# Optimization experiments

Measured on AMD Instinct MI355X. Metric: run time of the kernel, lower is better.

Reference implementation:

```python
import jax, jax.numpy as jnp
import numpy as np

D_MODEL = 1024
N_HEADS = 16
HEAD_DIM = D_MODEL // N_HEADS
FF_DIM = 4096
EPS = 1e-5


def _layer_norm(v, g, b):
    mu = jnp.mean(v, axis=-1, keepdims=True)
    var = jnp.mean(jnp.square(v - mu), axis=-1, keepdims=True)
    return (v - mu) * jax.lax.rsqrt(var + EPS) * g + b


def setup_inputs() -> dict:
    key = jax.random.key(0)
    ks = jax.random.split(key, 16)
    s = 0.02
    x = jax.random.normal(ks[0], (2, 2048, D_MODEL), dtype=jnp.float32)
    Wq = jax.random.normal(ks[1], (D_MODEL, D_MODEL), dtype=jnp.float32) * s
    Wk = jax.random.normal(ks[2], (D_MODEL, D_MODEL), dtype=jnp.float32) * s
    Wv = jax.random.normal(ks[3], (D_MODEL, D_MODEL), dtype=jnp.float32) * s
    Wo = jax.random.normal(ks[4], (D_MODEL, D_MODEL), dtype=jnp.float32) * s
    bq = jnp.zeros((D_MODEL,), jnp.float32)
    bk = jnp.zeros((D_MODEL,), jnp.float32)
    bv = jnp.zeros((D_MODEL,), jnp.float32)
    bo = jnp.zeros((D_MODEL,), jnp.float32)
    # per-head Conv1d(kernel=1) == per-head linear; weights [H, out, in]
    W1 = jax.random.normal(ks[5], (N_HEADS, FF_DIM, HEAD_DIM), dtype=jnp.float32) * s
    b1 = jnp.zeros((N_HEADS, FF_DIM), jnp.float32)
    W2 = jax.random.normal(ks[6], (N_HEADS, HEAD_DIM, FF_DIM), dtype=jnp.float32) * s
    b2 = jnp.zeros((N_HEADS, HEAD_DIM), jnp.float32)
    g1 = jnp.ones((D_MODEL,), jnp.float32)
    be1 = jnp.zeros((D_MODEL,), jnp.float32)
    g2 = jnp.ones((D_MODEL,), jnp.float32)
    be2 = jnp.zeros((D_MODEL,), jnp.float32)
    return {"x": x, "Wq": Wq, "bq": bq, "Wk": Wk, "bk": bk, "Wv": Wv, "bv": bv,
            "Wo": Wo, "bo": bo, "W1": W1, "b1": b1, "W2": W2, "b2": b2,
            "g1": g1, "be1": be1, "g2": g2, "be2": be2}


def reference(x, Wq, bq, Wk, bk, Wv, bv, Wo, bo, W1, b1, W2, b2, g1, be1, g2, be2):
    B, S, D = x.shape
    H, hd = N_HEADS, HEAD_DIM
    # --- multi-head self-attention (standard scaled dot-product) ---
    q = (x @ Wq + bq).reshape(B, S, H, hd)
    k = (x @ Wk + bk).reshape(B, S, H, hd)
    v = (x @ Wv + bv).reshape(B, S, H, hd)
    scores = jnp.einsum('bqhd,bkhd->bhqk', q, k) / jnp.sqrt(jnp.float32(hd))
    attn = jax.nn.softmax(scores, axis=-1)          # [B,H,S,S]
    ctx = jnp.einsum('bhqk,bkhd->bqhd', attn, v).reshape(B, S, D)
    residual = ctx @ Wo + bo
    # dropout is identity in eval mode
    x1 = _layer_norm(x + residual, g1, be1)
    # --- per-head feed-forward (Conv1d kernel=1 per head, batched over heads) ---
    xh = x1.reshape(B, S, H, hd)
    h = jax.nn.relu(jnp.einsum('bshd,hfd->bshf', xh, W1) + b1)   # [B,S,H,FF]
    ff = jnp.einsum('bshf,hdf->bshd', h, W2) + b2                 # [B,S,H,hd]
    y = _layer_norm(x1 + ff.reshape(B, S, D), g2, be2)
    return (y, attn)
```

## Files before the change

kernel.cpp:

```cpp
#include <hip/hip_runtime.h>
#include <cstddef>

#define D_M 1024
#define NH 16
#define HD 64
#define FFD 4096
#define SQ 2048
#define BB 2
#define TOK (BB*SQ)
#define EPS 1e-5f

typedef __attribute__((ext_vector_type(8))) short bf16x8;
typedef __attribute__((ext_vector_type(4))) float f32x4;

__device__ inline unsigned short f32_bf16_rne(float f) {
  unsigned int u = __float_as_uint(f);
  unsigned int r = (u + 0x7fffu + ((u >> 16) & 1u)) >> 16;
  return (unsigned short)r;
}

__device__ inline float wave_sum(float v) {
  #pragma unroll
  for (int m = 32; m >= 1; m >>= 1) v += __shfl_xor(v, m);
  return v;
}

__global__ __launch_bounds__(256)
void convert_bf16_k(const float* __restrict__ src, unsigned short* __restrict__ dst, int n4) {
  int i = blockIdx.x * 256 + threadIdx.x;
  if (i >= n4) return;
  float4 v = ((const float4*)src)[i];
  ushort4 h;
  h.x = f32_bf16_rne(v.x); h.y = f32_bf16_rne(v.y);
  h.z = f32_bf16_rne(v.z); h.w = f32_bf16_rne(v.w);
  ((ushort4*)dst)[i] = h;
}

__global__ __launch_bounds__(256)
void transp4_k(const float* __restrict__ W0, const float* __restrict__ W1_,
               const float* __restrict__ W2_, const float* __restrict__ W3,
               unsigned short* __restrict__ h0, unsigned short* __restrict__ h1,
               unsigned short* __restrict__ h2, unsigned short* __restrict__ h3) {
  const float* W; unsigned short* hT;
  switch (blockIdx.z) {
    case 0: W = W0; hT = h0; break;
    case 1: W = W1_; hT = h1; break;
    case 2: W = W2_; hT = h2; break;
    default: W = W3; hT = h3; break;
  }
  __shared__ float tile[64][65];
  const int bn = blockIdx.x * 64;
  const int bk = blockIdx.y * 64;
  const int t = threadIdx.x;
  #pragma unroll
  for (int i = 0; i < 4; ++i) {
    int r = (t >> 4) + i * 16, c = (t & 15) * 4;
    float4 v = *(const float4*)&W[(size_t)(bk + r) * D_M + bn + c];
    tile[r][c] = v.x; tile[r][c + 1] = v.y; tile[r][c + 2] = v.z; tile[r][c + 3] = v.w;
  }
  __syncthreads();
  #pragma unroll
  for (int i = 0; i < 4; ++i) {
    int n = (t >> 4) + i * 16, k = (t & 15) * 4;
    ushort4 h;
    h.x = f32_bf16_rne(tile[k][n]);     h.y = f32_bf16_rne(tile[k + 1][n]);
    h.z = f32_bf16_rne(tile[k + 2][n]); h.w = f32_bf16_rne(tile[k + 3][n]);
    *(ushort4*)&hT[(size_t)(bn + n) * D_M + bk + k] = h;
  }
}

__global__ __launch_bounds__(256)
void qkv_gemm_k(const unsigned short* __restrict__ xh_g,
                const unsigned short* __restrict__ Bqh, const unsigned short* __restrict__ Bkh,
                const unsigned short* __restrict__ Bvh,
                const float* __restrict__ bq, const float* __restrict__ bk, const float* __restrict__ bv,
                unsigned short* __restrict__ qh, unsigned short* __restrict__ kh,
                unsigned short* __restrict__ vth) {
  constexpr int LDK = 40;
  __shared__ unsigned short Ah[64 * LDK];
  __shared__ unsigned short Bh[3][128 * LDK];
  const int tid = threadIdx.x;
  const int wave = tid >> 6, lane = tid & 63;
  const int wm = (wave >> 1) * 32, wn = (wave & 1) * 64;
  const int bn = blockIdx.x * 128, bm = blockIdx.y * 64;
  const int K = D_M;

  f32x4 acc[3][2][4] = {};
  const int sr = tid >> 2, sk = (tid & 3) * 8;
  const int l15 = lane & 15, k8 = (lane >> 4) * 8;

  const unsigned short* Bhp[3] = {Bqh, Bkh, Bvh};

  for (int k0 = 0; k0 < K; k0 += 32) {
    *(uint4*)&Ah[sr * LDK + sk] = *(const uint4*)&xh_g[(size_t)(bm + sr) * K + k0 + sk];
    #pragma unroll
    for (int s = 0; s < 3; ++s) {
      #pragma unroll
      for (int c = 0; c < 2; ++c) {
        int r = sr + c * 64;
        *(uint4*)&Bh[s][r * LDK + sk] = *(const uint4*)&Bhp[s][(size_t)(bn + r) * K + k0 + sk];
      }
    }
    __syncthreads();
    bf16x8 af[2];
    #pragma unroll
    for (int m = 0; m < 2; ++m)
      af[m] = *(bf16x8*)&Ah[(wm + m * 16 + l15) * LDK + k8];
    #pragma unroll
    for (int s = 0; s < 3; ++s) {
      #pragma unroll
      for (int n = 0; n < 4; ++n) {
        bf16x8 b0 = *(bf16x8*)&Bh[s][(wn + n * 16 + l15) * LDK + k8];
        #pragma unroll
        for (int m = 0; m < 2; ++m) {
          if (s == 2) {
            acc[s][m][n] = __builtin_amdgcn_mfma_f32_16x16x32_bf16(af[m], b0, acc[s][m][n], 0, 0, 0);
          } else {
            acc[s][m][n] = __builtin_amdgcn_mfma_f32_16x16x32_bf16(b0, af[m], acc[s][m][n], 0, 0, 0);
          }
        }
      }
    }
    __syncthreads();
  }
  const int kq4 = (lane >> 4) * 4;
  #pragma unroll
  for (int s = 0; s < 2; ++s) {
    const float* bias = (s == 0) ? bq : bk;
    unsigned short* oh = (s == 0) ? qh : kh;
    #pragma unroll
    for (int n = 0; n < 4; ++n) {
      int colb = bn + wn + n * 16 + kq4;
      float4 bv4 = *(const float4*)&bias[colb];
      #pragma unroll
      for (int m = 0; m < 2; ++m) {
        int tok = bm + wm + m * 16 + l15;
        ushort4 h;
        h.x = f32_bf16_rne(acc[s][m][n][0] + bv4.x);
        h.y = f32_bf16_rne(acc[s][m][n][1] + bv4.y);
        h.z = f32_bf16_rne(acc[s][m][n][2] + bv4.z);
        h.w = f32_bf16_rne(acc[s][m][n][3] + bv4.w);
        *(ushort4*)&oh[(size_t)tok * D_M + colb] = h;
      }
    }
  }
  #pragma unroll
  for (int n = 0; n < 4; ++n) {
    int col = bn + wn + n * 16 + l15;
    float bvv = bv[col];
    #pragma unroll
    for (int m = 0; m < 2; ++m) {
      int row0 = bm + wm + m * 16 + kq4;
      ushort4 hv;
      hv.x = f32_bf16_rne(acc[2][m][n][0] + bvv); hv.y = f32_bf16_rne(acc[2][m][n][1] + bvv);
      hv.z = f32_bf16_rne(acc[2][m][n][2] + bvv); hv.w = f32_bf16_rne(acc[2][m][n][3] + bvv);
      size_t idx = (((size_t)(row0 >> 11) * NH + (col >> 6)) * HD + (col & 63)) * SQ + (row0 & 2047);
      *(ushort4*)&vth[idx] = hv;
    }
  }
}

__global__ __launch_bounds__(256)
void proj_gemm_k(const unsigned short* __restrict__ Ah_g,
                 const unsigned short* __restrict__ Bh_g,
                 const float* __restrict__ bias, float* __restrict__ C,
                 int M, int N, int K) {
  constexpr int LDK = 40;
  __shared__ unsigned short Ah[64 * LDK];
  __shared__ unsigned short Bh[128 * LDK];
  const int tid = threadIdx.x;
  const int wave = tid >> 6, lane = tid & 63;
  const int wm = (wave >> 1) * 32, wn = (wave & 1) * 64;
  const int bn = blockIdx.x * 128, bm = blockIdx.y * 64;

  f32x4 acc[2][4] = {};
  const int sr = tid >> 2, sk = (tid & 3) * 8;
  const int l15 = lane & 15, k8 = (lane >> 4) * 8;

  for (int k0 = 0; k0 < K; k0 += 32) {
    *(uint4*)&Ah[sr * LDK + sk] = *(const uint4*)&Ah_g[(size_t)(bm + sr) * K + k0 + sk];
    #pragma unroll
    for (int c = 0; c < 2; ++c) {
      int r = sr + c * 64;
      *(uint4*)&Bh[r * LDK + sk] = *(const uint4*)&Bh_g[(size_t)(bn + r) * K + k0 + sk];
    }
    __syncthreads();
    bf16x8 af[2], bfr[4];
    #pragma unroll
    for (int m = 0; m < 2; ++m)
      af[m] = *(bf16x8*)&Ah[(wm + m * 16 + l15) * LDK + k8];
    #pragma unroll
    for (int n = 0; n < 4; ++n)
      bfr[n] = *(bf16x8*)&Bh[(wn + n * 16 + l15) * LDK + k8];
    #pragma unroll
    for (int m = 0; m < 2; ++m)
      #pragma unroll
      for (int n = 0; n < 4; ++n)
        acc[m][n] = __builtin_amdgcn_mfma_f32_16x16x32_bf16(bfr[n], af[m], acc[m][n], 0, 0, 0);
    __syncthreads();
  }
  const int kq4 = (lane >> 4) * 4;
  #pragma unroll
  for (int n = 0; n < 4; ++n) {
    int colb = bn + wn + n * 16 + kq4;
    float4 bv4 = *(const float4*)&bias[colb];
    #pragma unroll
    for (int m = 0; m < 2; ++m) {
      int tok = bm + wm + m * 16 + l15;
      float4 v = {acc[m][n][0] + bv4.x, acc[m][n][1] + bv4.y,
                  acc[m][n][2] + bv4.z, acc[m][n][3] + bv4.w};
      *(float4*)&C[(size_t)tok * N + colb] = v;
    }
  }
}

__global__ __launch_bounds__(256)
void fused_attn_k(const unsigned short* __restrict__ qh,
                  const unsigned short* __restrict__ kh,
                  const unsigned short* __restrict__ vth,
                  float* __restrict__ attn,
                  unsigned short* __restrict__ ctxh) {
  constexpr int LDK = 72;
  constexpr int NT = SQ / 64;
  __shared__ unsigned short Kth[2][64 * LDK], Vts[2][64 * LDK];
  __shared__ unsigned short Ph[128 * LDK];
  const int tid = threadIdx.x, wave = tid >> 6, lane = tid & 63;
  const int l15 = lane & 15, kq = lane >> 4;
  const int bh = blockIdx.x, b = bh >> 4;
  const int h = bh & 15;
  const int q0 = blockIdx.y * 128;

  bf16x8 qfh[2][2];
  #pragma unroll
  for (int qi = 0; qi < 2; ++qi) {
    const size_t qoff = (size_t)(b * SQ + q0 + wave * 32 + qi * 16 + l15) * D_M + h * HD + kq * 8;
    qfh[qi][0] = *(const bf16x8*)&qh[qoff];  qfh[qi][1] = *(const bf16x8*)&qh[qoff + 32];
  }

  const size_t kbase = (size_t)(b * SQ) * D_M + h * HD;
  const size_t vbase = (size_t)bh * HD * SQ;
  const int srow = tid >> 2, sc = (tid & 3) * 16;

  float lsum[2] = {0.f, 0.f};
  {
    const unsigned short* src = &kh[kbase + (size_t)srow * D_M + sc];
    *(uint4*)&Kth[0][srow * LDK + sc] = *(const uint4*)src;
    *(uint4*)&Kth[0][srow * LDK + sc + 8] = *(const uint4*)(src + 8);
  }
  __syncthreads();
  for (int t = 0; t < NT; ++t) {
    const int cur = t & 1;
    const bool pf = (t + 1 < NT);
    uint4 r0, r1;
    if (pf) {
      const unsigned short* src = &kh[kbase + (size_t)((t + 1) * 64 + srow) * D_M + sc];
      r0 = *(const uint4*)src;
      r1 = *(const uint4*)(src + 8);
    }
    #pragma unroll
    for (int n = 0; n < 4; ++n) {
      bf16x8 kb0 = *(bf16x8*)&Kth[cur][(n * 16 + l15) * LDK + kq * 8];
      bf16x8 kb1 = *(bf16x8*)&Kth[cur][(n * 16 + l15) * LDK + 32 + kq * 8];
      #pragma unroll
      for (int qi = 0; qi < 2; ++qi) {
        f32x4 s = {};
        s = __builtin_amdgcn_mfma_f32_16x16x32_bf16(kb0, qfh[qi][0], s, 0, 0, 0);
        s = __builtin_amdgcn_mfma_f32_16x16x32_bf16(kb1, qfh[qi][1], s, 0, 0, 0);
        #pragma unroll
        for (int r = 0; r < 4; ++r) lsum[qi] += __expf(s[r] * 0.125f);
      }
    }
    if (pf) {
      *(uint4*)&Kth[cur ^ 1][srow * LDK + sc] = r0;
      *(uint4*)&Kth[cur ^ 1][srow * LDK + sc + 8] = r1;
    }
    __syncthreads();
  }
  float invl[2];
  #pragma unroll
  for (int qi = 0; qi < 2; ++qi) {
    float l = lsum[qi];
    l += __shfl_xor(l, 16);
    l += __shfl_xor(l, 32);
    invl[qi] = 1.0f / l;
  }

  f32x4 cacc[2][4] = {};
  {
    const unsigned short* srch = &kh[kbase + (size_t)srow * D_M + sc];
    const unsigned short* srcv = &vth[vbase + (size_t)srow * SQ + sc];
    *(uint4*)&Kth[0][srow * LDK + sc] = *(const uint4*)srch;
    *(uint4*)&Kth[0][srow * LDK + sc + 8] = *(const uint4*)(srch + 8);
    *(uint4*)&Vts[0][srow * LDK + sc] = *(const uint4*)srcv;
    *(uint4*)&Vts[0][srow * LDK + sc + 8] = *(const uint4*)(srcv + 8);
  }
  __syncthreads();
  for (int t = 0; t < NT; ++t) {
    const int cur = t & 1;
    const int k0 = t * 64;
    const bool pf = (t + 1 < NT);
    uint4 rk0, rk1, rv0, rv1;
    if (pf) {
      const unsigned short* srch = &kh[kbase + (size_t)(k0 + 64 + srow) * D_M + sc];
      const unsigned short* srcv = &vth[vbase + (size_t)srow * SQ + k0 + 64 + sc];
      rk0 = *(const uint4*)srch; rk1 = *(const uint4*)(srch + 8);
      rv0 = *(const uint4*)srcv; rv1 = *(const uint4*)(srcv + 8);
    }
    #pragma unroll
    for (int n = 0; n < 4; ++n) {
      bf16x8 kb0 = *(bf16x8*)&Kth[cur][(n * 16 + l15) * LDK + kq * 8];
      bf16x8 kb1 = *(bf16x8*)&Kth[cur][(n * 16 + l15) * LDK + 32 + kq * 8];
      #pragma unroll
      for (int qi = 0; qi < 2; ++qi) {
        f32x4 s = {};
        s = __builtin_amdgcn_mfma_f32_16x16x32_bf16(kb0, qfh[qi][0], s, 0, 0, 0);
        s = __builtin_amdgcn_mfma_f32_16x16x32_bf16(kb1, qfh[qi][1], s, 0, 0, 0);
        float4 pv;
        pv.x = __expf(s[0] * 0.125f) * invl[qi];
        pv.y = __expf(s[1] * 0.125f) * invl[qi];
        pv.z = __expf(s[2] * 0.125f) * invl[qi];
        pv.w = __expf(s[3] * 0.125f) * invl[qi];
        const int qrow = wave * 32 + qi * 16 + l15;
        *(float4*)&attn[((size_t)bh * SQ + q0 + qrow) * SQ + k0 + n * 16 + kq * 4] = pv;
        ushort4 p4;
        p4.x = f32_bf16_rne(pv.x); p4.y = f32_bf16_rne(pv.y);
        p4.z = f32_bf16_rne(pv.z); p4.w = f32_bf16_rne(pv.w);
        *(ushort4*)&Ph[qrow * LDK + n * 16 + kq * 4] = p4;
      }
    }
    __syncthreads();
    #pragma unroll
    for (int qi = 0; qi < 2; ++qi) {
      bf16x8 pa0 = *(bf16x8*)&Ph[(wave * 32 + qi * 16 + l15) * LDK + kq * 8];
      bf16x8 pa1 = *(bf16x8*)&Ph[(wave * 32 + qi * 16 + l15) * LDK + 32 + kq * 8];
      #pragma unroll
      for (int n = 0; n < 4; ++n) {
        bf16x8 vb0 = *(bf16x8*)&Vts[cur][(n * 16 + l15) * LDK + kq * 8];
        bf16x8 vb1 = *(bf16x8*)&Vts[cur][(n * 16 + l15) * LDK + 32 + kq * 8];
        cacc[qi][n] = __builtin_amdgcn_mfma_f32_16x16x32_bf16(vb0, pa0, cacc[qi][n], 0, 0, 0);
        cacc[qi][n] = __builtin_amdgcn_mfma_f32_16x16x32_bf16(vb1, pa1, cacc[qi][n], 0, 0, 0);
      }
    }
    if (pf) {
      *(uint4*)&Kth[cur ^ 1][srow * LDK + sc] = rk0;
      *(uint4*)&Kth[cur ^ 1][srow * LDK + sc + 8] = rk1;
      *(uint4*)&Vts[cur ^ 1][srow * LDK + sc] = rv0;
      *(uint4*)&Vts[cur ^ 1][srow * LDK + sc + 8] = rv1;
    }
    __syncthreads();
  }
  #pragma unroll
  for (int qi = 0; qi < 2; ++qi)
    #pragma unroll
    for (int n = 0; n < 4; ++n) {
      ushort4 hh;
      hh.x = f32_bf16_rne(cacc[qi][n][0]); hh.y = f32_bf16_rne(cacc[qi][n][1]);
      hh.z = f32_bf16_rne(cacc[qi][n][2]); hh.w = f32_bf16_rne(cacc[qi][n][3]);
      size_t off = (size_t)(b * SQ + q0 + wave * 32 + qi * 16 + l15) * D_M + h * HD + n * 16 + kq * 4;
      *(ushort4*)&ctxh[off] = hh;
    }
}

__global__ __launch_bounds__(256)
void ff_bf16_k(const unsigned short* __restrict__ x1h,
               const unsigned short* __restrict__ W1h_, const float* __restrict__ b1,
               const unsigned short* __restrict__ W2h_, const float* __restrict__ b2,
               float* __restrict__ out) {
  constexpr int LDW = 72;
  constexpr int LDH = 40;
  __shared__ unsigned short W1sh[2][32 * LDW];
  __shared__ unsigned short W2sh[2][64 * LDH];
  __shared__ unsigned short Hh[128 * LDH];

  const int tid = threadIdx.x;
  const int wave = tid >> 6, lane = tid & 63;
  const int wm = wave >> 1, wf = wave & 1, wd = wave & 1;
  const int h = blockIdx.x;
  const int m0 = blockIdx.y * 128;
  const int l15 = lane & 15, kq = lane >> 4;

  const size_t w1base = (size_t)h * FFD * HD;
  const size_t w2base = (size_t)h * HD * FFD;
  const int r1 = tid >> 3, k1 = (tid & 7) * 8;
  const int r2 = tid >> 2, f2 = (tid & 3) * 8;

  bf16x8 xf[4][2];
  #pragma unroll
  for (int m = 0; m < 4; ++m)
    #pragma unroll
    for (int ks = 0; ks < 2; ++ks) {
      size_t gof = (size_t)(m0 + wm * 64 + m * 16 + l15) * D_M + h * HD + ks * 32 + kq * 8;
      xf[m][ks] = *(const bf16x8*)&x1h[gof];
    }

  {
    *(uint4*)&W1sh[0][r1 * LDW + k1] = *(const uint4*)&W1h_[w1base + (size_t)r1 * HD + k1];
    *(uint4*)&W2sh[0][r2 * LDH + f2] = *(const uint4*)&W2h_[w2base + (size_t)r2 * FFD + f2];
  }
  __syncthreads();

  f32x4 ffacc[4][2] = {};

  for (int ch = 0; ch < FFD / 32; ++ch) {
    const int buf = ch & 1;
    const bool pf = (ch + 1 < FFD / 32);
    uint4 w1h_r, w2h_r;
    if (pf) {
      const int f0n = (ch + 1) * 32;
      w1h_r = *(const uint4*)&W1h_[w1base + (size_t)(f0n + r1) * HD + k1];
      w2h_r = *(const uint4*)&W2h_[w2base + (size_t)r2 * FFD + f0n + f2];
    }
    f32x4 hacc[4] = {};
    #pragma unroll
    for (int ks = 0; ks < 2; ++ks) {
      bf16x8 w1h = *(bf16x8*)&W1sh[buf][(wf * 16 + l15) * LDW + ks * 32 + kq * 8];
      #pragma unroll
      for (int m = 0; m < 4; ++m)
        hacc[m] = __builtin_amdgcn_mfma_f32_16x16x32_bf16(w1h, xf[m][ks], hacc[m], 0, 0, 0);
    }
    {
      const int fb = wf * 16 + kq * 4;
      float4 b1v = *(const float4*)&b1[(size_t)h * FFD + ch * 32 + fb];
      const float bb[4] = {b1v.x, b1v.y, b1v.z, b1v.w};
      #pragma unroll
      for (int m = 0; m < 4; ++m) {
        int tok = wm * 64 + m * 16 + l15;
        ushort4 hh;
        hh.x = f32_bf16_rne(fmaxf(hacc[m][0] + bb[0], 0.0f));
        hh.y = f32_bf16_rne(fmaxf(hacc[m][1] + bb[1], 0.0f));
        hh.z = f32_bf16_rne(fmaxf(hacc[m][2] + bb[2], 0.0f));
        hh.w = f32_bf16_rne(fmaxf(hacc[m][3] + bb[3], 0.0f));
        *(ushort4*)&Hh[tok * LDH + fb] = hh;
      }
    }
    __syncthreads();
    bf16x8 hfr[4];
    #pragma unroll
    for (int m = 0; m < 4; ++m)
      hfr[m] = *(bf16x8*)&Hh[(wm * 64 + m * 16 + l15) * LDH + kq * 8];
    #pragma unroll
    for (int n = 0; n < 2; ++n) {
      bf16x8 w2h = *(bf16x8*)&W2sh[buf][(wd * 32 + n * 16 + l15) * LDH + kq * 8];
      #pragma unroll
      for (int m = 0; m < 4; ++m)
        ffacc[m][n] = __builtin_amdgcn_mfma_f32_16x16x32_bf16(w2h, hfr[m], ffacc[m][n], 0, 0, 0);
    }
    if (pf) {
      *(uint4*)&W1sh[buf ^ 1][r1 * LDW + k1] = w1h_r;
      *(uint4*)&W2sh[buf ^ 1][r2 * LDH + f2] = w2h_r;
    }
    __syncthreads();
  }
  #pragma unroll
  for (int n = 0; n < 2; ++n) {
    int db = wd * 32 + n * 16 + kq * 4;
    float4 b2v = *(const float4*)&b2[(size_t)h * HD + db];
    #pragma unroll
    for (int m = 0; m < 4; ++m) {
      int tok = m0 + wm * 64 + m * 16 + l15;
      float4 v = {ffacc[m][n][0] + b2v.x, ffacc[m][n][1] + b2v.y,
                  ffacc[m][n][2] + b2v.z, ffacc[m][n][3] + b2v.w};
      *(float4*)&out[(size_t)tok * D_M + h * HD + db] = v;
    }
  }
}

template<int BF16OUT>
__global__ __launch_bounds__(256)
void add_ln_kernel(const float* __restrict__ a, const float* __restrict__ r,
                   const float* __restrict__ g, const float* __restrict__ be,
                   float* __restrict__ out, unsigned short* __restrict__ oh) {
  const size_t row = blockIdx.x;
  const int tid = threadIdx.x;
  __shared__ float red1[4];
  __shared__ float red2[4];
  float4 va = ((const float4*)(a + row * D_M))[tid];
  float4 vr = ((const float4*)(r + row * D_M))[tid];
  float v0 = va.x + vr.x, v1 = va.y + vr.y, v2 = va.z + vr.z, v3 = va.w + vr.w;
  float s = v0 + v1 + v2 + v3;
  float sq = v0 * v0 + v1 * v1 + v2 * v2 + v3 * v3;
  s = wave_sum(s);
  sq = wave_sum(sq);
  if ((tid & 63) == 0) { red1[tid >> 6] = s; red2[tid >> 6] = sq; }
  __syncthreads();
  s = red1[0] + red1[1] + red1[2] + red1[3];
  sq = red2[0] + red2[1] + red2[2] + red2[3];
  const float mu = s * (1.0f / D_M);
  const float var = sq * (1.0f / D_M) - mu * mu;
  float x = var + EPS;
  float rs = rsqrtf(x);
  rs = rs * (1.5f - 0.5f * x * rs * rs);
  float4 gg = ((const float4*)g)[tid];
  float4 bb = ((const float4*)be)[tid];
  float4 o = {(v0 - mu) * rs * gg.x + bb.x, (v1 - mu) * rs * gg.y + bb.y,
              (v2 - mu) * rs * gg.z + bb.z, (v3 - mu) * rs * gg.w + bb.w};
  ((float4*)(out + row * D_M))[tid] = o;
  if (BF16OUT) {
    ushort4 h;
    h.x = f32_bf16_rne(o.x); h.y = f32_bf16_rne(o.y);
    h.z = f32_bf16_rne(o.z); h.w = f32_bf16_rne(o.w);
    ((ushort4*)(oh + row * D_M))[tid] = h;
  }
}

extern "C" void kernel_launch(void* const* d_in, const int* in_sizes, int n_in,
                              void* d_out, int out_size, void* d_ws, size_t ws_size,
                              hipStream_t stream) {
  const float* x   = (const float*)d_in[0];
  const float* Wq  = (const float*)d_in[1];
  const float* bq  = (const float*)d_in[2];
  const float* Wk  = (const float*)d_in[3];
  const float* bk  = (const float*)d_in[4];
  const float* Wv  = (const float*)d_in[5];
  const float* bv  = (const float*)d_in[6];
  const float* Wo  = (const float*)d_in[7];
  const float* bo  = (const float*)d_in[8];
  const float* W1  = (const float*)d_in[9];
  const float* b1  = (const float*)d_in[10];
  const float* W2  = (const float*)d_in[11];
  const float* b2  = (const float*)d_in[12];
  const float* g1  = (const float*)d_in[13];
  const float* be1 = (const float*)d_in[14];
  const float* g2  = (const float*)d_in[15];
  const float* be2 = (const float*)d_in[16];

  float* y_out = (float*)d_out;
  float* attn  = (float*)d_out + (size_t)TOK * D_M;

  char* p = (char*)d_ws;
  const size_t MB = 1024 * 1024;
  unsigned short* WqT = (unsigned short*)(p + 0 * MB);
  unsigned short* WkT = (unsigned short*)(p + 2 * MB);
  unsigned short* WvT = (unsigned short*)(p + 4 * MB);
  unsigned short* WoT = (unsigned short*)(p + 6 * MB);
  unsigned short* xh  = (unsigned short*)(p + 8 * MB);
  unsigned short* qh  = (unsigned short*)(p + 16 * MB);
  unsigned short* kh  = (unsigned short*)(p + 24 * MB);
  unsigned short* vth = (unsigned short*)(p + 32 * MB);
  unsigned short* ctxh = (unsigned short*)(p + 40 * MB);
  float* resid = (float*)(p + 48 * MB);
  float* x1b   = (float*)(p + 64 * MB);
  unsigned short* x1c_h = (unsigned short*)(p + 8 * MB);
  unsigned short* W1c_h = (unsigned short*)(p + 16 * MB);
  unsigned short* W2c_h = (unsigned short*)(p + 24 * MB);
  float* ffb = (float*)(p + 32 * MB);

  const dim3 blk(256);
  const int n4_act = TOK * D_M / 4;

  transp4_k<<<dim3(16, 16, 4), blk, 0, stream>>>(Wq, Wk, Wv, Wo, WqT, WkT, WvT, WoT);
  convert_bf16_k<<<dim3(n4_act / 256), blk, 0, stream>>>(x, xh, n4_act);

  qkv_gemm_k<<<dim3(D_M / 128, TOK / 64), blk, 0, stream>>>(
      xh, WqT, WkT, WvT, bq, bk, bv, qh, kh, vth);

  fused_attn_k<<<dim3(BB * NH, SQ / 128), blk, 0, stream>>>(qh, kh, vth, attn, ctxh);

  proj_gemm_k<<<dim3(D_M / 128, TOK / 64), blk, 0, stream>>>(
      ctxh, WoT, bo, resid, TOK, D_M, D_M);
  add_ln_kernel<1><<<dim3(TOK), blk, 0, stream>>>(x, resid, g1, be1, x1b, x1c_h);

  convert_bf16_k<<<dim3(n4_act / 256), blk, 0, stream>>>(W1, W1c_h, n4_act);
  convert_bf16_k<<<dim3(n4_act / 256), blk, 0, stream>>>(W2, W2c_h, n4_act);
  ff_bf16_k<<<dim3(NH, TOK / 128), blk, 0, stream>>>(x1c_h, W1c_h, b1, W2c_h, b2, ffb);
  add_ln_kernel<0><<<dim3(TOK), blk, 0, stream>>>(x1b, ffb, g2, be2, y_out, nullptr);
}
```

Measured before the change: 493.2 us.

## Drop LDS staging in attention kernel, load K/V fragments directly from global

```diff
diff --git a/kernel.cpp b/kernel.cpp
--- a/kernel.cpp
+++ b/kernel.cpp
@@ -220,145 +220,79 @@
                   const unsigned short* __restrict__ vth,
                   float* __restrict__ attn,
                   unsigned short* __restrict__ ctxh) {
-  constexpr int LDK = 72;
-  constexpr int NT = SQ / 64;
-  __shared__ unsigned short Kth[2][64 * LDK], Vts[2][64 * LDK];
-  __shared__ unsigned short Ph[128 * LDK];
+  constexpr int LDP = 72;
+  __shared__ unsigned short Ph[64 * LDP];
   const int tid = threadIdx.x, wave = tid >> 6, lane = tid & 63;
   const int l15 = lane & 15, kq = lane >> 4;
-  const int bh = blockIdx.x, b = bh >> 4;
-  const int h = bh & 15;
-  const int q0 = blockIdx.y * 128;
-
-  bf16x8 qfh[2][2];
-  #pragma unroll
-  for (int qi = 0; qi < 2; ++qi) {
-    const size_t qoff = (size_t)(b * SQ + q0 + wave * 32 + qi * 16 + l15) * D_M + h * HD + kq * 8;
-    qfh[qi][0] = *(const bf16x8*)&qh[qoff];  qfh[qi][1] = *(const bf16x8*)&qh[qoff + 32];
-  }
+  const int bh = blockIdx.x, b = bh >> 4, h = bh & 15;
+  const int q0 = blockIdx.y * 64;
+
+  const size_t qoff = (size_t)(b * SQ + q0 + wave * 16 + l15) * D_M + h * HD + kq * 8;
+  const bf16x8 qf0 = *(const bf16x8*)&qh[qoff];
+  const bf16x8 qf1 = *(const bf16x8*)&qh[qoff + 32];
 
   const size_t kbase = (size_t)(b * SQ) * D_M + h * HD;
   const size_t vbase = (size_t)bh * HD * SQ;
-  const int srow = tid >> 2, sc = (tid & 3) * 16;
-
-  float lsum[2] = {0.f, 0.f};
-  {
-    const unsigned short* src = &kh[kbase + (size_t)srow * D_M + sc];
-    *(uint4*)&Kth[0][srow * LDK + sc] = *(const uint4*)src;
-    *(uint4*)&Kth[0][srow * LDK + sc + 8] = *(const uint4*)(src + 8);
-  }
-  __syncthreads();
-  for (int t = 0; t < NT; ++t) {
-    const int cur = t & 1;
-    const bool pf = (t + 1 < NT);
-    uint4 r0, r1;
-    if (pf) {
-      const unsigned short* src = &kh[kbase + (size_t)((t + 1) * 64 + srow) * D_M + sc];
-      r0 = *(const uint4*)src;
-      r1 = *(const uint4*)(src + 8);
-    }
+
+  float lsum = 0.f;
+  for (int k0 = 0; k0 < SQ; k0 += 64) {
     #pragma unroll
     for (int n = 0; n < 4; ++n) {
-      bf16x8 kb0 = *(bf16x8*)&Kth[cur][(n * 16 + l15) * LDK + kq * 8];
-      bf16x8 kb1 = *(bf16x8*)&Kth[cur][(n * 16 + l15) * LDK + 32 + kq * 8];
-      #pragma unroll
-      for (int qi = 0; qi < 2; ++qi) {
-        f32x4 s = {};
-        s = __builtin_amdgcn_mfma_f32_16x16x32_bf16(kb0, qfh[qi][0], s, 0, 0, 0);
-        s = __builtin_amdgcn_mfma_f32_16x16x32_bf16(kb1, qfh[qi][1], s, 0, 0, 0);
-        #pragma unroll
-        for (int r = 0; r < 4; ++r) lsum[qi] += __expf(s[r] * 0.125f);
-      }
-    }
-    if (pf) {
-      *(uint4*)&Kth[cur ^ 1][srow * LDK + sc] = r0;
-      *(uint4*)&Kth[cur ^ 1][srow * LDK + sc + 8] = r1;
-    }
-    __syncthreads();
-  }
-  float invl[2];
-  #pragma unroll
-  for (int qi = 0; qi < 2; ++qi) {
-    float l = lsum[qi];
-    l += __shfl_xor(l, 16);
-    l += __shfl_xor(l, 32);
-    invl[qi] = 1.0f / l;
-  }
-
-  f32x4 cacc[2][4] = {};
-  {
-    const unsigned short* srch = &kh[kbase + (size_t)srow * D_M + sc];
-    const unsigned short* srcv = &vth[vbase + (size_t)srow * SQ + sc];
-    *(uint4*)&Kth[0][srow * LDK + sc] = *(const uint4*)srch;
-    *(uint4*)&Kth[0][srow * LDK + sc + 8] = *(const uint4*)(srch + 8);
-    *(uint4*)&Vts[0][srow * LDK + sc] = *(const uint4*)srcv;
-    *(uint4*)&Vts[0][srow * LDK + sc + 8] = *(const uint4*)(srcv + 8);
-  }
-  __syncthreads();
-  for (int t = 0; t < NT; ++t) {
-    const int cur = t & 1;
-    const int k0 = t * 64;
-    const bool pf = (t + 1 < NT);
-    uint4 rk0, rk1, rv0, rv1;
-    if (pf) {
-      const unsigned short* srch = &kh[kbase + (size_t)(k0 + 64 + srow) * D_M + sc];
-      const unsigned short* srcv = &vth[vbase + (size_t)srow * SQ + k0 + 64 + sc];
-      rk0 = *(const uint4*)srch; rk1 = *(const uint4*)(srch + 8);
-      rv0 = *(const uint4*)srcv; rv1 = *(const uint4*)(srcv + 8);
-    }
+      const unsigned short* kr = &kh[kbase + (size_t)(k0 + n * 16 + l15) * D_M + kq * 8];
+      bf16x8 kb0 = *(const bf16x8*)kr;
+      bf16x8 kb1 = *(const bf16x8*)(kr + 32);
+      f32x4 s = {};
+      s = __builtin_amdgcn_mfma_f32_16x16x32_bf16(kb0, qf0, s, 0, 0, 0);
+      s = __builtin_amdgcn_mfma_f32_16x16x32_bf16(kb1, qf1, s, 0, 0, 0);
+      #pragma unroll
+      for (int r = 0; r < 4; ++r) lsum += __expf(s[r] * 0.125f);
+    }
+  }
+  lsum += __shfl_xor(lsum, 16);
+  lsum += __shfl_xor(lsum, 32);
+  const float invl = 1.0f / lsum;
+
+  f32x4 cacc[4] = {};
+  const size_t arow = ((size_t)bh * SQ + q0 + wave * 16 + l15) * SQ;
+  for (int k0 = 0; k0 < SQ; k0 += 64) {
     #pragma unroll
     for (int n = 0; n < 4; ++n) {
-      bf16x8 kb0 = *(bf16x8*)&Kth[cur][(n * 16 + l15) * LDK + kq * 8];
-      bf16x8 kb1 = *(bf16x8*)&Kth[cur][(n * 16 + l15) * LDK + 32 + kq * 8];
-      #pragma unroll
-      for (int qi = 0; qi < 2; ++qi) {
-        f32x4 s = {};
-        s = __builtin_amdgcn_mfma_f32_16x16x32_bf16(kb0, qfh[qi][0], s, 0, 0, 0);
-        s = __builtin_amdgcn_mfma_f32_16x16x32_bf16(kb1, qfh[qi][1], s, 0, 0, 0);
-        float4 pv;
-        pv.x = __expf(s[0] * 0.125f) * invl[qi];
-        pv.y = __expf(s[1] * 0.125f) * invl[qi];
-        pv.z = __expf(s[2] * 0.125f) * invl[qi];
-        pv.w = __expf(s[3] * 0.125f) * invl[qi];
-        const int qrow = wave * 32 + qi * 16 + l15;
-        *(float4*)&attn[((size_t)bh * SQ + q0 + qrow) * SQ + k0 + n * 16 + kq * 4] = pv;
-        ushort4 p4;
-        p4.x = f32_bf16_rne(pv.x); p4.y = f32_bf16_rne(pv.y);
-        p4.z = f32_bf16_rne(pv.z); p4.w = f32_bf16_rne(pv.w);
-        *(ushort4*)&Ph[qrow * LDK + n * 16 + kq * 4] = p4;
-      }
-    }
-    __syncthreads();
-    #pragma unroll
-    for (int qi = 0; qi < 2; ++qi) {
-      bf16x8 pa0 = *(bf16x8*)&Ph[(wave * 32 + qi * 16 + l15) * LDK + kq * 8];
-      bf16x8 pa1 = *(bf16x8*)&Ph[(wave * 32 + qi * 16 + l15) * LDK + 32 + kq * 8];
-      #pragma unroll
-      for (int n = 0; n < 4; ++n) {
-        bf16x8 vb0 = *(bf16x8*)&Vts[cur][(n * 16 + l15) * LDK + kq * 8];
-        bf16x8 vb1 = *(bf16x8*)&Vts[cur][(n * 16 + l15) * LDK + 32 + kq * 8];
-        cacc[qi][n] = __builtin_amdgcn_mfma_f32_16x16x32_bf16(vb0, pa0, cacc[qi][n], 0, 0, 0);
-        cacc[qi][n] = __builtin_amdgcn_mfma_f32_16x16x32_bf16(vb1, pa1, cacc[qi][n], 0, 0, 0);
-      }
-    }
-    if (pf) {
-      *(uint4*)&Kth[cur ^ 1][srow * LDK + sc] = rk0;
-      *(uint4*)&Kth[cur ^ 1][srow * LDK + sc + 8] = rk1;
-      *(uint4*)&Vts[cur ^ 1][srow * LDK + sc] = rv0;
-      *(uint4*)&Vts[cur ^ 1][srow * LDK + sc + 8] = rv1;
-    }
-    __syncthreads();
-  }
-  #pragma unroll
-  for (int qi = 0; qi < 2; ++qi)
+      const unsigned short* kr = &kh[kbase + (size_t)(k0 + n * 16 + l15) * D_M + kq * 8];
+      bf16x8 kb0 = *(const bf16x8*)kr;
+      bf16x8 kb1 = *(const bf16x8*)(kr + 32);
+      f32x4 s = {};
+      s = __builtin_amdgcn_mfma_f32_16x16x32_bf16(kb0, qf0, s, 0, 0, 0);
+      s = __builtin_amdgcn_mfma_f32_16x16x32_bf16(kb1, qf1, s, 0, 0, 0);
+      float4 pv;
+      pv.x = __expf(s[0] * 0.125f) * invl;
+      pv.y = __expf(s[1] * 0.125f) * invl;
+      pv.z = __expf(s[2] * 0.125f) * invl;
+      pv.w = __expf(s[3] * 0.125f) * invl;
+      *(float4*)&attn[arow + k0 + n * 16 + kq * 4] = pv;
+      ushort4 p4;
+      p4.x = f32_bf16_rne(pv.x); p4.y = f32_bf16_rne(pv.y);
+      p4.z = f32_bf16_rne(pv.z); p4.w = f32_bf16_rne(pv.w);
+      *(ushort4*)&Ph[(wave * 16 + l15) * LDP + n * 16 + kq * 4] = p4;
+    }
+    bf16x8 pa0 = *(bf16x8*)&Ph[(wave * 16 + l15) * LDP + kq * 8];
+    bf16x8 pa1 = *(bf16x8*)&Ph[(wave * 16 + l15) * LDP + 32 + kq * 8];
     #pragma unroll
     for (int n = 0; n < 4; ++n) {
-      ushort4 hh;
-      hh.x = f32_bf16_rne(cacc[qi][n][0]); hh.y = f32_bf16_rne(cacc[qi][n][1]);
-      hh.z = f32_bf16_rne(cacc[qi][n][2]); hh.w = f32_bf16_rne(cacc[qi][n][3]);
-      size_t off = (size_t)(b * SQ + q0 + wave * 32 + qi * 16 + l15) * D_M + h * HD + n * 16 + kq * 4;
-      *(ushort4*)&ctxh[off] = hh;
-    }
+      const unsigned short* vr = &vth[vbase + (size_t)(n * 16 + l15) * SQ + k0 + kq * 8];
+      bf16x8 vb0 = *(const bf16x8*)vr;
+      bf16x8 vb1 = *(const bf16x8*)(vr + 32);
+      cacc[n] = __builtin_amdgcn_mfma_f32_16x16x32_bf16(vb0, pa0, cacc[n], 0, 0, 0);
+      cacc[n] = __builtin_amdgcn_mfma_f32_16x16x32_bf16(vb1, pa1, cacc[n], 0, 0, 0);
+    }
+  }
+  #pragma unroll
+  for (int n = 0; n < 4; ++n) {
+    ushort4 hh;
+    hh.x = f32_bf16_rne(cacc[n][0]); hh.y = f32_bf16_rne(cacc[n][1]);
+    hh.z = f32_bf16_rne(cacc[n][2]); hh.w = f32_bf16_rne(cacc[n][3]);
+    size_t off = (size_t)(b * SQ + q0 + wave * 16 + l15) * D_M + h * HD + n * 16 + kq * 4;
+    *(ushort4*)&ctxh[off] = hh;
+  }
 }
 
 __global__ __launch_bounds__(256)
@@ -554,7 +488,7 @@
   qkv_gemm_k<<<dim3(D_M / 128, TOK / 64), blk, 0, stream>>>(
       xh, WqT, WkT, WvT, bq, bk, bv, qh, kh, vth);
 
-  fused_attn_k<<<dim3(BB * NH, SQ / 128), blk, 0, stream>>>(qh, kh, vth, attn, ctxh);
+  fused_attn_k<<<dim3(BB * NH, SQ / 64), blk, 0, stream>>>(qh, kh, vth, attn, ctxh);
 
   proj_gemm_k<<<dim3(D_M / 128, TOK / 64), blk, 0, stream>>>(
       ctxh, WoT, bo, resid, TOK, D_M, D_M);
```

Result: slower. 626.9 us (+27.1%).
